# Optimization experiments

Hardware: AMD Instinct MI355X
Metric: run time of the kernel (lower is better)

## Reference

```python
import jax, jax.numpy as jnp
import numpy as np

N = 50000          # nodes
E = 1600000        # edges (avg degree 32)
H, DH = 8, 16      # heads, dim per head (SE3Transformer heads=8, dim_head=16)
D_IN = 8           # pos(3) + node-type embedding(5)
EDGE_DIM = 4       # edge_attr features (num_degrees=4)
HID = H * DH       # 128 = hidden_dim
OUT = 1
TYPES = 100
GRAPHS = 64


def setup_inputs() -> dict:
    key = jax.random.key(0)
    ks = jax.random.split(key, 12)
    pos = jax.random.normal(ks[0], (N, 3), dtype=jnp.float32)
    z = jax.random.randint(ks[1], (N,), 0, TYPES)
    edge_index = jax.random.randint(ks[2], (2, E), 0, N)
    edge_attr = jax.random.normal(ks[3], (E, EDGE_DIM), dtype=jnp.float32)
    batch = jnp.sort(jax.random.randint(ks[4], (N,), 0, GRAPHS))
    s = 0.1
    emb = jax.random.normal(ks[5], (TYPES, D_IN - 3), dtype=jnp.float32) * s
    Wq = jax.random.normal(ks[6], (D_IN, HID), dtype=jnp.float32) * s
    Wk = jax.random.normal(ks[7], (D_IN + EDGE_DIM, HID), dtype=jnp.float32) * s
    Wv = jax.random.normal(ks[8], (D_IN + EDGE_DIM, HID), dtype=jnp.float32) * s
    Wo = jax.random.normal(ks[9], (HID, HID), dtype=jnp.float32) * s
    lin_W = jax.random.normal(ks[10], (HID, OUT), dtype=jnp.float32) * s
    lin_b = jnp.zeros((OUT,), dtype=jnp.float32)
    return {"pos": pos, "z": z, "edge_index": edge_index, "edge_attr": edge_attr,
            "batch": batch, "emb": emb, "Wq": Wq, "Wk": Wk, "Wv": Wv,
            "Wo": Wo, "lin_W": lin_W, "lin_b": lin_b}


def reference(pos, z, edge_index, edge_attr, batch, emb, Wq, Wk, Wv, Wo, lin_W, lin_b):
    # node features: concat(pos, embedding(z))  -> [N, 8]
    x = jnp.concatenate([pos, emb[z]], axis=-1)
    src, dst = edge_index[0], edge_index[1]

    # edge-indexed multi-head graph attention (SE3Transformer core pattern)
    q = (x @ Wq).reshape(N, H, DH)                           # [N, H, DH]
    e_in = jnp.concatenate([x[src], edge_attr], axis=-1)     # [E, 12] gather
    k = (e_in @ Wk).reshape(E, H, DH)
    v = (e_in @ Wv).reshape(E, H, DH)

    scale = 1.0 / jnp.sqrt(jnp.float32(DH))
    scores = jnp.einsum('ehd,ehd->eh', q[dst], k) * scale    # [E, H]

    # segment softmax over incoming edges of each destination node
    m = jax.ops.segment_max(scores, dst, num_segments=N)     # [N, H]
    ex = jnp.exp(scores - m[dst])
    denom = jax.ops.segment_sum(ex, dst, num_segments=N)     # [N, H]
    w = ex / jnp.maximum(denom[dst], 1e-9)                   # [E, H]

    agg = jax.ops.segment_sum(w[:, :, None] * v, dst, num_segments=N)  # [N, H, DH]
    feats = agg.reshape(N, HID) @ Wo                         # [N, 128]

    h = jax.nn.relu(feats)
    y = h @ lin_W + lin_b                                    # [N, OUT]

    # global mean pool per graph
    sums = jax.ops.segment_sum(y, batch, num_segments=GRAPHS)
    cnts = jax.ops.segment_sum(jnp.ones((N, 1), y.dtype), batch, num_segments=GRAPHS)
    return sums / jnp.maximum(cnts, 1.0)                     # [GRAPHS, OUT]
```

## Files before the change

### kernel.cpp

```cpp
#include <hip/hip_runtime.h>

#define N_NODES 50000
#define N_EDGES 1600000
#define NHEAD 8
#define DH 16
#define D_IN 8
#define E_IN_DIM 12
#define HID 128
#define GRAPHS 64
#define N_PAD 50016
#define BINK 98
#define NB 512
#define T_MS 2048
#define MSB ((N_EDGES + T_MS - 1) / T_MS)
#define LCAP 3840

__global__ __launch_bounds__(256) void k_node1(
    const float* __restrict__ pos, const int* __restrict__ z,
    const float* __restrict__ emb,
    const float* __restrict__ Wq, const float* __restrict__ Wk,
    float* __restrict__ x, float* __restrict__ qk)
{
    __shared__ float sWq[D_IN * HID];
    __shared__ float sWk[E_IN_DIM * HID];
    __shared__ float sx[32][D_IN];

    int tid = threadIdx.x;
    for (int i = tid; i < D_IN * HID; i += 256) sWq[i] = Wq[i];
    for (int i = tid; i < E_IN_DIM * HID; i += 256) sWk[i] = Wk[i];

    int nl = tid >> 3;
    int h  = tid & 7;
    int n  = blockIdx.x * 32 + nl;

    if (n < N_NODES) {
        int j = h;
        float v;
        if (j < 3) v = pos[n * 3 + j];
        else       v = emb[z[n] * 5 + (j - 3)];
        sx[nl][j] = v;
        x[n * D_IN + j] = v;
    }
    __syncthreads();
    if (n >= N_NODES) return;

    float q[DH];
    #pragma unroll
    for (int d = 0; d < DH; ++d) {
        float acc = 0.f;
        #pragma unroll
        for (int j = 0; j < D_IN; ++j)
            acc += sx[nl][j] * sWq[j * HID + h * DH + d];
        q[d] = acc;
    }
    const float scale = 0.25f;
    #pragma unroll
    for (int j = 0; j < E_IN_DIM; ++j) {
        float acc = 0.f;
        #pragma unroll
        for (int d = 0; d < DH; ++d)
            acc += q[d] * sWk[j * HID + h * DH + d];
        qk[n * 96 + h * 12 + j] = acc * scale;
    }
}

__global__ __launch_bounds__(256) void k_bhist(
    const int* __restrict__ dst, int* __restrict__ bcount)
{
    __shared__ int lh[NB];
    int tid = threadIdx.x;
    for (int i = tid; i < NB; i += 256) lh[i] = 0;
    __syncthreads();

    int stride = gridDim.x * 256;
    const int NI4 = N_EDGES / 4;
    for (int i = blockIdx.x * 256 + tid; i < NI4; i += stride) {
        int4 d4 = ((const int4*)dst)[i];
        atomicAdd(&lh[d4.x / BINK], 1);
        atomicAdd(&lh[d4.y / BINK], 1);
        atomicAdd(&lh[d4.z / BINK], 1);
        atomicAdd(&lh[d4.w / BINK], 1);
    }
    __syncthreads();
    for (int i = tid; i < NB; i += 256) {
        int v = lh[i];
        if (v > 0) atomicAdd(&bcount[i * 16], v);
    }
}

__global__ __launch_bounds__(512) void k_bscan(
    const int* __restrict__ bcount, int* __restrict__ binoff, int* __restrict__ bincur)
{
    __shared__ int tmp[NB];
    int t = threadIdx.x;
    int v = bcount[t * 16];
    tmp[t] = v;
    __syncthreads();
    #pragma unroll
    for (int off = 1; off < NB; off <<= 1) {
        int u = (t >= off) ? tmp[t - off] : 0;
        __syncthreads();
        if (t >= off) tmp[t] += u;
        __syncthreads();
    }
    int ex = tmp[t] - v;
    binoff[t] = ex;
    bincur[t * 16] = ex;
    if (t == NB - 1) binoff[NB] = tmp[t];
}

__global__ __launch_bounds__(512) void k_msplit(
    const int* __restrict__ edge_index, const float* __restrict__ edge_attr,
    int* __restrict__ bincur,
    int2* __restrict__ sd_g, float4* __restrict__ ea_g)
{
    __shared__ int    hist[NB];
    __shared__ int    hscan[NB];
    __shared__ int    gb[NB];
    __shared__ int2   ssd[T_MS];
    __shared__ float4 sea[T_MS];
    __shared__ int    dest[T_MS];

    int tid = threadIdx.x;
    int base = blockIdx.x * T_MS;
    int nact = min(T_MS, N_EDGES - base);

    hist[tid] = 0;
    __syncthreads();

    int e0 = base + tid * 4;
    bool act = (e0 + 4) <= N_EDGES;
    int srcs[4], dsts[4], myb[4], myr[4];
    float4 eav[4];
    if (act) {
        int4 sa = *(const int4*)(edge_index + e0);
        int4 da = *(const int4*)(edge_index + N_EDGES + e0);
        srcs[0]=sa.x; srcs[1]=sa.y; srcs[2]=sa.z; srcs[3]=sa.w;
        dsts[0]=da.x; dsts[1]=da.y; dsts[2]=da.z; dsts[3]=da.w;
        const float4* ep = (const float4*)edge_attr + e0;
        eav[0] = ep[0]; eav[1] = ep[1]; eav[2] = ep[2]; eav[3] = ep[3];
        #pragma unroll
        for (int k = 0; k < 4; ++k) {
            myb[k] = dsts[k] / BINK;
            myr[k] = atomicAdd(&hist[myb[k]], 1);
        }
    }
    __syncthreads();

    int v = hist[tid];
    hscan[tid] = v;
    __syncthreads();
    #pragma unroll
    for (int off = 1; off < NB; off <<= 1) {
        int u = (tid >= off) ? hscan[tid - off] : 0;
        __syncthreads();
        if (tid >= off) hscan[tid] += u;
        __syncthreads();
    }
    int ex = hscan[tid] - v;
    int g = 0;
    if (v > 0) g = atomicAdd(&bincur[tid * 16], v);
    hscan[tid] = ex;
    gb[tid] = g;
    __syncthreads();

    if (act) {
        #pragma unroll
        for (int k = 0; k < 4; ++k) {
            int li = hscan[myb[k]] + myr[k];
            ssd[li]  = make_int2(srcs[k], dsts[k]);
            sea[li]  = eav[k];
            dest[li] = gb[myb[k]] + myr[k];
        }
    }
    __syncthreads();

    for (int i = tid; i < nact; i += 512) {
        int d = dest[i];
        sd_g[d] = ssd[i];
        ea_g[d] = sea[i];
    }
}

__global__ __launch_bounds__(512) void k_attn_f(
    const int* __restrict__ binoff, const int2* __restrict__ sd_g,
    const float4* __restrict__ ea_g,
    const float* __restrict__ x,
    const float* __restrict__ qk, const float* __restrict__ Wv,
    float* __restrict__ agg)
{
    __shared__ float sWv[E_IN_DIM * HID];
    __shared__ int   soff[129];
    __shared__ int   cnt[BINK];
    __shared__ int   stmp[128];
    __shared__ int2  list[LCAP];

    int tid = threadIdx.x;
    int b = blockIdx.x;
    int nlo = b * BINK;
    int nhi = min(nlo + BINK, N_NODES);
    int nn = nhi - nlo;
    if (nn <= 0) return;

    for (int i = tid; i < E_IN_DIM * HID; i += 512) sWv[i] = Wv[i];
    for (int i = tid; i < nn; i += 512) cnt[i] = 0;
    int gbeg = binoff[b];
    int total = binoff[b + 1] - gbeg;
    __syncthreads();

    for (int i = tid; i < total; i += 512) {
        int2 v = sd_g[gbeg + i];
        atomicAdd(&cnt[v.y - nlo], 1);
    }
    __syncthreads();

    if (tid < 128) stmp[tid] = (tid < nn) ? cnt[tid] : 0;
    __syncthreads();
    #pragma unroll
    for (int off = 1; off < 128; off <<= 1) {
        int u = 0;
        if (tid < 128 && tid >= off) u = stmp[tid - off];
        __syncthreads();
        if (tid < 128 && tid >= off) stmp[tid] += u;
        __syncthreads();
    }
    if (tid < 128) soff[tid + 1] = stmp[tid];
    if (tid == 0) soff[0] = 0;
    for (int i = tid; i < nn; i += 512) cnt[i] = 0;
    __syncthreads();

    for (int i = tid; i < total; i += 512) {
        int2 v = sd_g[gbeg + i];
        int ln = v.y - nlo;
        int r = atomicAdd(&cnt[ln], 1);
        int li = soff[ln] + r;
        if (li < LCAP) list[li] = make_int2(v.x, i);
    }
    __syncthreads();

    int w = tid >> 6, l = tid & 63;
    int es = l >> 3, h = l & 7;
    const float4* easeg = ea_g + gbeg;
    for (int nl = w; nl < nn; nl += 8) {
        int n = nlo + nl;
        const float4* qr = (const float4*)(qk + (size_t)n * 96 + h * 12);
        float4 q0 = qr[0], q1 = qr[1], q2 = qr[2];
        int lbeg = soff[nl];
        int lcnt = soff[nl + 1] - lbeg;

        float sr[12];
        #pragma unroll
        for (int j = 0; j < 12; ++j) sr[j] = 0.f;
        float denom = 0.f;

        int umax = (lcnt + 7) >> 3;
        #pragma unroll 2
        for (int u = 0; u < umax; ++u) {
            int r = u * 8 + es;
            bool a2 = r < lcnt;
            int2 p = list[lbeg + (a2 ? r : 0)];
            const float4* xp = (const float4*)(x + p.x * 8);
            float4 x0 = xp[0], x1 = xp[1];
            float4 ea = easeg[p.y];
            float sc = x0.x*q0.x + x0.y*q0.y + x0.z*q0.z + x0.w*q0.w
                     + x1.x*q1.x + x1.y*q1.y + x1.z*q1.z + x1.w*q1.w
                     + ea.x*q2.x + ea.y*q2.y + ea.z*q2.z + ea.w*q2.w;
            float ex = a2 ? __expf(sc) : 0.f;
            denom += ex;
            sr[0] += ex * x0.x; sr[1]  += ex * x0.y; sr[2]  += ex * x0.z; sr[3]  += ex * x0.w;
            sr[4] += ex * x1.x; sr[5]  += ex * x1.y; sr[6]  += ex * x1.z; sr[7]  += ex * x1.w;
            sr[8] += ex * ea.x; sr[9]  += ex * ea.y; sr[10] += ex * ea.z; sr[11] += ex * ea.w;
        }

        #pragma unroll
        for (int m = 8; m <= 32; m <<= 1) {
            denom += __shfl_xor(denom, m);
            #pragma unroll
            for (int j = 0; j < 12; ++j) sr[j] += __shfl_xor(sr[j], m);
        }

        float inv = 1.0f / fmaxf(denom, 1e-9f);
        int d0 = h * DH + 2 * es;
        float a0 = 0.f, a1 = 0.f;
        #pragma unroll
        for (int j = 0; j < E_IN_DIM; ++j) {
            a0 += sr[j] * sWv[j * HID + d0];
            a1 += sr[j] * sWv[j * HID + d0 + 1];
        }
        *(float2*)(agg + (size_t)n * HID + d0) = make_float2(a0 * inv, a1 * inv);
    }
}

__global__ __launch_bounds__(256) void k_mlp(
    const float* __restrict__ agg, const float* __restrict__ Wo,
    const float* __restrict__ lin_W, const float* __restrict__ lin_b,
    const int* __restrict__ batch,
    float* __restrict__ gsum, float* __restrict__ gcnt)
{
    __shared__ float sWo[64 * HID];
    __shared__ float sAgg[32][HID + 1];
    __shared__ float sRed[8][33];
    __shared__ float bsum[GRAPHS];
    __shared__ int   bcnt[GRAPHS];

    int tid = threadIdx.x;
    int nbase = blockIdx.x * 32;

    if (tid < GRAPHS) { bsum[tid] = 0.f; bcnt[tid] = 0; }

    {
        const float4* ag = (const float4*)(agg + (size_t)nbase * HID);
        #pragma unroll
        for (int k = 0; k < 4; ++k) {
            int i4 = k * 256 + tid;
            float4 v = ag[i4];
            int fi = i4 * 4;
            int r = fi >> 7, c = fi & 127;
            sAgg[r][c] = v.x; sAgg[r][c + 1] = v.y; sAgg[r][c + 2] = v.z; sAgg[r][c + 3] = v.w;
        }
    }

    int h  = tid >> 5;
    int nl = tid & 31;
    int n  = nbase + nl;

    float f[16];
    #pragma unroll
    for (int d = 0; d < 16; ++d) f[d] = 0.f;

    #pragma unroll
    for (int half = 0; half < 2; ++half) {
        __syncthreads();
        const float4* wp = (const float4*)(Wo + half * 64 * HID);
        #pragma unroll
        for (int k = 0; k < 8; ++k) {
            int i4 = k * 256 + tid;
            ((float4*)sWo)[i4] = wp[i4];
        }
        __syncthreads();
        #pragma unroll 4
        for (int i = 0; i < 64; ++i) {
            float av = sAgg[nl][half * 64 + i];
            const float4* wr = (const float4*)(sWo + i * HID + h * 16);
            float4 w0 = wr[0], w1 = wr[1], w2 = wr[2], w3 = wr[3];
            f[0]  += av * w0.x; f[1]  += av * w0.y; f[2]  += av * w0.z; f[3]  += av * w0.w;
            f[4]  += av * w1.x; f[5]  += av * w1.y; f[6]  += av * w1.z; f[7]  += av * w1.w;
            f[8]  += av * w2.x; f[9]  += av * w2.y; f[10] += av * w2.z; f[11] += av * w2.w;
            f[12] += av * w3.x; f[13] += av * w3.y; f[14] += av * w3.z; f[15] += av * w3.w;
        }
    }

    const float4* lwp = (const float4*)(lin_W + h * 16);
    float4 lw0 = lwp[0], lw1 = lwp[1], lw2 = lwp[2], lw3 = lwp[3];
    float ps = fmaxf(f[0],0.f)*lw0.x + fmaxf(f[1],0.f)*lw0.y + fmaxf(f[2],0.f)*lw0.z + fmaxf(f[3],0.f)*lw0.w
             + fmaxf(f[4],0.f)*lw1.x + fmaxf(f[5],0.f)*lw1.y + fmaxf(f[6],0.f)*lw1.z + fmaxf(f[7],0.f)*lw1.w
             + fmaxf(f[8],0.f)*lw2.x + fmaxf(f[9],0.f)*lw2.y + fmaxf(f[10],0.f)*lw2.z + fmaxf(f[11],0.f)*lw2.w
             + fmaxf(f[12],0.f)*lw3.x + fmaxf(f[13],0.f)*lw3.y + fmaxf(f[14],0.f)*lw3.z + fmaxf(f[15],0.f)*lw3.w;

    sRed[h][nl] = ps;
    __syncthreads();
    if (h == 0 && n < N_NODES) {
        float y = lin_b[0];
        #pragma unroll
        for (int k = 0; k < 8; ++k) y += sRed[k][nl];
        int g = batch[n];
        atomicAdd(&bsum[g], y);
        atomicAdd(&bcnt[g], 1);
    }
    __syncthreads();
    if (tid < GRAPHS) {
        int c = bcnt[tid];
        if (c > 0) {
            atomicAdd(&gsum[tid], bsum[tid]);
            atomicAdd(&gcnt[tid], (float)c);
        }
    }
}

__global__ void k_final(const float* __restrict__ gsum, const float* __restrict__ gcnt,
                        float* __restrict__ out)
{
    int g = threadIdx.x;
    if (g < GRAPHS) out[g] = gsum[g] / fmaxf(gcnt[g], 1.0f);
}

extern "C" void kernel_launch(void* const* d_in, const int* in_sizes, int n_in,
                              void* d_out, int out_size, void* d_ws, size_t ws_size,
                              hipStream_t stream)
{
    const float* pos       = (const float*)d_in[0];
    const int*   z         = (const int*)  d_in[1];
    const int*   edge_index= (const int*)  d_in[2];
    const float* edge_attr = (const float*)d_in[3];
    const int*   batch     = (const int*)  d_in[4];
    const float* emb       = (const float*)d_in[5];
    const float* Wq        = (const float*)d_in[6];
    const float* Wk        = (const float*)d_in[7];
    const float* Wv        = (const float*)d_in[8];
    const float* Wo        = (const float*)d_in[9];
    const float* lin_W     = (const float*)d_in[10];
    const float* lin_b     = (const float*)d_in[11];
    float* out = (float*)d_out;

    char* ws = (char*)d_ws;
    float* gsum   = (float*)ws;
    float* gcnt   = gsum + GRAPHS;
    int*   bcount = (int*)(gcnt + GRAPHS);
    int*   binoff = bcount + NB * 16;
    int*   bincur = binoff + 520;
    char*  tail   = (char*)(bincur + NB * 16);

    hipMemsetAsync(gsum, 0, (size_t)(2 * GRAPHS + NB * 16) * sizeof(int), stream);

    int2*   sd_g = (int2*)tail;
    float4* ea_g = (float4*)(sd_g + N_EDGES);
    float*  x    = (float*)(ea_g + N_EDGES);
    float*  qk   = x + (size_t)N_NODES * 8;
    float*  agg  = qk + (size_t)N_NODES * 96;

    k_node1 <<<(N_NODES + 31) / 32, 256, 0, stream>>>(pos, z, emb, Wq, Wk, x, qk);
    k_bhist <<<512, 256, 0, stream>>>(edge_index + N_EDGES, bcount);
    k_bscan <<<1, NB, 0, stream>>>(bcount, binoff, bincur);
    k_msplit<<<MSB, 512, 0, stream>>>(edge_index, edge_attr, bincur, sd_g, ea_g);
    k_attn_f<<<NB, 512, 0, stream>>>(binoff, sd_g, ea_g, x, qk, Wv, agg);
    k_mlp   <<<(N_PAD / 32), 256, 0, stream>>>(agg, Wo, lin_W, lin_b, batch, gsum, gcnt);
    k_final <<<1, 64, 0, stream>>>(gsum, gcnt, out);
}
```

Before: 190.2 us.

## Fuse q·Wk projection into attention kernel and widen blocks to 1024 threads

The per-node q and folded q·Wk vectors are now computed inside the attention kernel, one node per wavefront, instead of a separate node kernel writing a 96-float-per-node qk buffer to global memory. The node kernel shrinks to building x only. The attention kernel grows to 1024 threads with 16 wavefronts, and each thread keeps its edge records in registers between the counting pass and the list-building pass rather than reading them from global memory twice. The trade-off is extra per-node compute and shared-memory/register pressure in the attention kernel. The intra-wave shared-memory exchange relies on wavefront lockstep plus waitcnt rather than a barrier, and the held[4] buffer assumes at most 4096 edges per bin.

```diff
diff --git a/kernel.cpp b/kernel.cpp
--- a/kernel.cpp
+++ b/kernel.cpp
@@ -15,53 +15,18 @@
 #define MSB ((N_EDGES + T_MS - 1) / T_MS)
 #define LCAP 3840
 
-__global__ __launch_bounds__(256) void k_node1(
+__global__ __launch_bounds__(256) void k_nodex(
     const float* __restrict__ pos, const int* __restrict__ z,
-    const float* __restrict__ emb,
-    const float* __restrict__ Wq, const float* __restrict__ Wk,
-    float* __restrict__ x, float* __restrict__ qk)
-{
-    __shared__ float sWq[D_IN * HID];
-    __shared__ float sWk[E_IN_DIM * HID];
-    __shared__ float sx[32][D_IN];
-
-    int tid = threadIdx.x;
-    for (int i = tid; i < D_IN * HID; i += 256) sWq[i] = Wq[i];
-    for (int i = tid; i < E_IN_DIM * HID; i += 256) sWk[i] = Wk[i];
-
-    int nl = tid >> 3;
-    int h  = tid & 7;
-    int n  = blockIdx.x * 32 + nl;
-
-    if (n < N_NODES) {
-        int j = h;
-        float v;
-        if (j < 3) v = pos[n * 3 + j];
-        else       v = emb[z[n] * 5 + (j - 3)];
-        sx[nl][j] = v;
-        x[n * D_IN + j] = v;
-    }
-    __syncthreads();
+    const float* __restrict__ emb, float* __restrict__ x)
+{
+    int n = blockIdx.x * 256 + threadIdx.x;
     if (n >= N_NODES) return;
-
-    float q[DH];
-    #pragma unroll
-    for (int d = 0; d < DH; ++d) {
-        float acc = 0.f;
-        #pragma unroll
-        for (int j = 0; j < D_IN; ++j)
-            acc += sx[nl][j] * sWq[j * HID + h * DH + d];
-        q[d] = acc;
-    }
-    const float scale = 0.25f;
-    #pragma unroll
-    for (int j = 0; j < E_IN_DIM; ++j) {
-        float acc = 0.f;
-        #pragma unroll
-        for (int d = 0; d < DH; ++d)
-            acc += q[d] * sWk[j * HID + h * DH + d];
-        qk[n * 96 + h * 12 + j] = acc * scale;
-    }
+    float p0 = pos[n * 3], p1 = pos[n * 3 + 1], p2 = pos[n * 3 + 2];
+    const float* e = emb + z[n] * 5;
+    float e0 = e[0], e1 = e[1], e2 = e[2], e3 = e[3], e4 = e[4];
+    float4* xp = (float4*)(x + (size_t)n * 8);
+    xp[0] = make_float4(p0, p1, p2, e0);
+    xp[1] = make_float4(e1, e2, e3, e4);
 }
 
 __global__ __launch_bounds__(256) void k_bhist(
@@ -182,18 +147,23 @@
     }
 }
 
-__global__ __launch_bounds__(512) void k_attn_f(
+__global__ __launch_bounds__(1024) void k_attn_f(
     const int* __restrict__ binoff, const int2* __restrict__ sd_g,
     const float4* __restrict__ ea_g,
     const float* __restrict__ x,
-    const float* __restrict__ qk, const float* __restrict__ Wv,
+    const float* __restrict__ Wq, const float* __restrict__ Wk,
+    const float* __restrict__ Wv,
     float* __restrict__ agg)
 {
     __shared__ float sWv[E_IN_DIM * HID];
+    __shared__ float sWq[D_IN * HID];
+    __shared__ float sWk[E_IN_DIM * HID];
     __shared__ int   soff[129];
     __shared__ int   cnt[BINK];
     __shared__ int   stmp[128];
     __shared__ int2  list[LCAP];
+    __shared__ float qsc[16][128];
+    __shared__ float qksc[16][96];
 
     int tid = threadIdx.x;
     int b = blockIdx.x;
@@ -202,15 +172,22 @@
     int nn = nhi - nlo;
     if (nn <= 0) return;
 
-    for (int i = tid; i < E_IN_DIM * HID; i += 512) sWv[i] = Wv[i];
-    for (int i = tid; i < nn; i += 512) cnt[i] = 0;
+    for (int i = tid; i < E_IN_DIM * HID; i += 1024) sWv[i] = Wv[i];
+    for (int i = tid; i < D_IN * HID; i += 1024) sWq[i] = Wq[i];
+    for (int i = tid; i < E_IN_DIM * HID; i += 1024) sWk[i] = Wk[i];
+    for (int i = tid; i < nn; i += 1024) cnt[i] = 0;
     int gbeg = binoff[b];
     int total = binoff[b + 1] - gbeg;
     __syncthreads();
 
-    for (int i = tid; i < total; i += 512) {
-        int2 v = sd_g[gbeg + i];
-        atomicAdd(&cnt[v.y - nlo], 1);
+    int2 held[4];
+    #pragma unroll
+    for (int k = 0; k < 4; ++k) {
+        int i = tid + k * 1024;
+        if (i < total) {
+            held[k] = sd_g[gbeg + i];
+            atomicAdd(&cnt[held[k].y - nlo], 1);
+        }
     }
     __syncthreads();
 
@@ -226,25 +203,61 @@
     }
     if (tid < 128) soff[tid + 1] = stmp[tid];
     if (tid == 0) soff[0] = 0;
-    for (int i = tid; i < nn; i += 512) cnt[i] = 0;
-    __syncthreads();
-
-    for (int i = tid; i < total; i += 512) {
-        int2 v = sd_g[gbeg + i];
-        int ln = v.y - nlo;
-        int r = atomicAdd(&cnt[ln], 1);
-        int li = soff[ln] + r;
-        if (li < LCAP) list[li] = make_int2(v.x, i);
+    for (int i = tid; i < nn; i += 1024) cnt[i] = 0;
+    __syncthreads();
+
+    #pragma unroll
+    for (int k = 0; k < 4; ++k) {
+        int i = tid + k * 1024;
+        if (i < total) {
+            int ln = held[k].y - nlo;
+            int r = atomicAdd(&cnt[ln], 1);
+            int li = soff[ln] + r;
+            if (li < LCAP) list[li] = make_int2(held[k].x, i);
+        }
     }
     __syncthreads();
 
     int w = tid >> 6, l = tid & 63;
     int es = l >> 3, h = l & 7;
     const float4* easeg = ea_g + gbeg;
-    for (int nl = w; nl < nn; nl += 8) {
+    for (int nl = w; nl < nn; nl += 16) {
         int n = nlo + nl;
-        const float4* qr = (const float4*)(qk + (size_t)n * 96 + h * 12);
+
+        {
+            const float4* xp4 = (const float4*)(x + (size_t)n * 8);
+            float4 xa = xp4[0], xb = xp4[1];
+            float xr[8] = {xa.x, xa.y, xa.z, xa.w, xb.x, xb.y, xb.z, xb.w};
+            float qa = 0.f, qb = 0.f;
+            #pragma unroll
+            for (int j = 0; j < 8; ++j) {
+                qa += xr[j] * sWq[j * HID + 2 * l];
+                qb += xr[j] * sWq[j * HID + 2 * l + 1];
+            }
+            qsc[w][2 * l]     = qa;
+            qsc[w][2 * l + 1] = qb;
+            __builtin_amdgcn_s_waitcnt(0);
+            {
+                int e = l, hh = e / 12, jj = e % 12;
+                float acc = 0.f;
+                #pragma unroll
+                for (int d = 0; d < 16; ++d)
+                    acc += qsc[w][hh * 16 + d] * sWk[jj * HID + hh * 16 + d];
+                qksc[w][e] = acc * 0.25f;
+                if (l < 32) {
+                    int e2 = l + 64, h2 = e2 / 12, j2 = e2 % 12;
+                    float acc2 = 0.f;
+                    #pragma unroll
+                    for (int d = 0; d < 16; ++d)
+                        acc2 += qsc[w][h2 * 16 + d] * sWk[j2 * HID + h2 * 16 + d];
+                    qksc[w][e2] = acc2 * 0.25f;
+                }
+            }
+            __builtin_amdgcn_s_waitcnt(0);
+        }
+        const float4* qr = (const float4*)&qksc[w][h * 12];
         float4 q0 = qr[0], q1 = qr[1], q2 = qr[2];
+
         int lbeg = soff[nl];
         int lcnt = soff[nl + 1] - lbeg;
 
@@ -415,14 +428,13 @@
     int2*   sd_g = (int2*)tail;
     float4* ea_g = (float4*)(sd_g + N_EDGES);
     float*  x    = (float*)(ea_g + N_EDGES);
-    float*  qk   = x + (size_t)N_NODES * 8;
-    float*  agg  = qk + (size_t)N_NODES * 96;
-
-    k_node1 <<<(N_NODES + 31) / 32, 256, 0, stream>>>(pos, z, emb, Wq, Wk, x, qk);
+    float*  agg  = x + (size_t)N_NODES * 8;
+
+    k_nodex <<<(N_NODES + 255) / 256, 256, 0, stream>>>(pos, z, emb, x);
     k_bhist <<<512, 256, 0, stream>>>(edge_index + N_EDGES, bcount);
     k_bscan <<<1, NB, 0, stream>>>(bcount, binoff, bincur);
     k_msplit<<<MSB, 512, 0, stream>>>(edge_index, edge_attr, bincur, sd_g, ea_g);
-    k_attn_f<<<NB, 512, 0, stream>>>(binoff, sd_g, ea_g, x, qk, Wv, agg);
+    k_attn_f<<<NB, 1024, 0, stream>>>(binoff, sd_g, ea_g, x, Wq, Wk, Wv, agg);
     k_mlp   <<<(N_PAD / 32), 256, 0, stream>>>(agg, Wo, lin_W, lin_b, batch, gsum, gcnt);
     k_final <<<1, 64, 0, stream>>>(gsum, gcnt, out);
 }
```

Result: no change. 193.0 us (+1.4%).

## Split each attention bin across two blocks and cache edge records in registers

Applied to the files above, without the earlier changes.

The attention kernel now launches two blocks per destination-node bin, each handling half of the bin's nodes (49 nodes) with a smaller shared edge list. Each block scans its parent bin's edges and keeps only the ones landing in its half. Those edge records are held in registers between the counting pass and the list-building pass instead of being read from global memory twice. The aim is more blocks in flight and lower shared memory per block, at the cost of each block reading the whole parent bin. It also assumes no bin holds more than 4096 edges.

```diff
diff --git a/kernel.cpp b/kernel.cpp
--- a/kernel.cpp
+++ b/kernel.cpp
@@ -11,9 +11,11 @@
 #define N_PAD 50016
 #define BINK 98
 #define NB 512
+#define SBK 49
+#define NSUB 1024
 #define T_MS 2048
 #define MSB ((N_EDGES + T_MS - 1) / T_MS)
-#define LCAP 3840
+#define LCAP 2048
 
 __global__ __launch_bounds__(256) void k_node1(
     const float* __restrict__ pos, const int* __restrict__ z,
@@ -190,51 +192,63 @@
     float* __restrict__ agg)
 {
     __shared__ float sWv[E_IN_DIM * HID];
-    __shared__ int   soff[129];
-    __shared__ int   cnt[BINK];
-    __shared__ int   stmp[128];
+    __shared__ int   soff[SBK + 1];
+    __shared__ int   cnt[SBK];
+    __shared__ int   stmp[64];
     __shared__ int2  list[LCAP];
 
     int tid = threadIdx.x;
     int b = blockIdx.x;
-    int nlo = b * BINK;
-    int nhi = min(nlo + BINK, N_NODES);
+    int parent = b >> 1;
+    int nlo = parent * BINK + (b & 1) * SBK;
+    int nhi = min(nlo + SBK, N_NODES);
     int nn = nhi - nlo;
     if (nn <= 0) return;
 
     for (int i = tid; i < E_IN_DIM * HID; i += 512) sWv[i] = Wv[i];
     for (int i = tid; i < nn; i += 512) cnt[i] = 0;
-    int gbeg = binoff[b];
-    int total = binoff[b + 1] - gbeg;
-    __syncthreads();
-
-    for (int i = tid; i < total; i += 512) {
-        int2 v = sd_g[gbeg + i];
-        atomicAdd(&cnt[v.y - nlo], 1);
-    }
-    __syncthreads();
-
-    if (tid < 128) stmp[tid] = (tid < nn) ? cnt[tid] : 0;
-    __syncthreads();
-    #pragma unroll
-    for (int off = 1; off < 128; off <<= 1) {
+    int gbeg = binoff[parent];
+    int total = binoff[parent + 1] - gbeg;
+    __syncthreads();
+
+    int2 held[8];
+    #pragma unroll
+    for (int k = 0; k < 8; ++k) {
+        int i = tid + k * 512;
+        if (i < total) {
+            held[k] = sd_g[gbeg + i];
+            int ln = held[k].y - nlo;
+            if (ln >= 0 && ln < nn) atomicAdd(&cnt[ln], 1);
+        }
+    }
+    __syncthreads();
+
+    if (tid < 64) stmp[tid] = (tid < nn) ? cnt[tid] : 0;
+    __syncthreads();
+    #pragma unroll
+    for (int off = 1; off < 64; off <<= 1) {
         int u = 0;
-        if (tid < 128 && tid >= off) u = stmp[tid - off];
-        __syncthreads();
-        if (tid < 128 && tid >= off) stmp[tid] += u;
-        __syncthreads();
-    }
-    if (tid < 128) soff[tid + 1] = stmp[tid];
+        if (tid < 64 && tid >= off) u = stmp[tid - off];
+        __syncthreads();
+        if (tid < 64 && tid >= off) stmp[tid] += u;
+        __syncthreads();
+    }
+    if (tid < 64) soff[tid + 1] = stmp[tid];
     if (tid == 0) soff[0] = 0;
     for (int i = tid; i < nn; i += 512) cnt[i] = 0;
     __syncthreads();
 
-    for (int i = tid; i < total; i += 512) {
-        int2 v = sd_g[gbeg + i];
-        int ln = v.y - nlo;
-        int r = atomicAdd(&cnt[ln], 1);
-        int li = soff[ln] + r;
-        if (li < LCAP) list[li] = make_int2(v.x, i);
+    #pragma unroll
+    for (int k = 0; k < 8; ++k) {
+        int i = tid + k * 512;
+        if (i < total) {
+            int ln = held[k].y - nlo;
+            if (ln >= 0 && ln < nn) {
+                int r = atomicAdd(&cnt[ln], 1);
+                int li = soff[ln] + r;
+                if (li < LCAP) list[li] = make_int2(held[k].x, i);
+            }
+        }
     }
     __syncthreads();
 
@@ -422,7 +436,7 @@
     k_bhist <<<512, 256, 0, stream>>>(edge_index + N_EDGES, bcount);
     k_bscan <<<1, NB, 0, stream>>>(bcount, binoff, bincur);
     k_msplit<<<MSB, 512, 0, stream>>>(edge_index, edge_attr, bincur, sd_g, ea_g);
-    k_attn_f<<<NB, 512, 0, stream>>>(binoff, sd_g, ea_g, x, qk, Wv, agg);
+    k_attn_f<<<NSUB, 512, 0, stream>>>(binoff, sd_g, ea_g, x, qk, Wv, agg);
     k_mlp   <<<(N_PAD / 32), 256, 0, stream>>>(agg, Wo, lin_W, lin_b, batch, gsum, gcnt);
     k_final <<<1, 64, 0, stream>>>(gsum, gcnt, out);
 }
```

New measurement: 196.3 us. 3.2% more time.

## Enlarge msplit tiles and scatter via LDS permutation instead of staged payload

Applied to the files above, without the earlier changes.

The edge-partition kernel now handles 8192 edges per block with 1024 threads, so each bin's global run per block is longer and fewer atomics hit the global bin cursors. Instead of staging the src/dst and edge_attr payload in LDS, it keeps only dst values plus a 16-bit permutation, then re-reads src and edge_attr from global memory in bin-sorted order when writing. This cuts LDS footprint and should make the global writes more contiguous, at the cost of scattered global re-reads of the payload and fewer, larger blocks.

```diff
diff --git a/kernel.cpp b/kernel.cpp
--- a/kernel.cpp
+++ b/kernel.cpp
@@ -11,7 +11,7 @@
 #define N_PAD 50016
 #define BINK 98
 #define NB 512
-#define T_MS 2048
+#define T_MS 8192
 #define MSB ((N_EDGES + T_MS - 1) / T_MS)
 #define LCAP 3840
 
@@ -109,76 +109,65 @@
     if (t == NB - 1) binoff[NB] = tmp[t];
 }
 
-__global__ __launch_bounds__(512) void k_msplit(
+__global__ __launch_bounds__(1024) void k_msplit(
     const int* __restrict__ edge_index, const float* __restrict__ edge_attr,
     int* __restrict__ bincur,
     int2* __restrict__ sd_g, float4* __restrict__ ea_g)
 {
-    __shared__ int    hist[NB];
-    __shared__ int    hscan[NB];
-    __shared__ int    gb[NB];
-    __shared__ int2   ssd[T_MS];
-    __shared__ float4 sea[T_MS];
-    __shared__ int    dest[T_MS];
+    __shared__ int hist[NB];
+    __shared__ int hscan[NB];
+    __shared__ int cnt[NB];
+    __shared__ int gb[NB];
+    __shared__ int stmp[NB];
+    __shared__ int sdst[T_MS];
+    __shared__ unsigned short perm[T_MS];
 
     int tid = threadIdx.x;
     int base = blockIdx.x * T_MS;
     int nact = min(T_MS, N_EDGES - base);
-
-    hist[tid] = 0;
-    __syncthreads();
-
-    int e0 = base + tid * 4;
-    bool act = (e0 + 4) <= N_EDGES;
-    int srcs[4], dsts[4], myb[4], myr[4];
-    float4 eav[4];
-    if (act) {
-        int4 sa = *(const int4*)(edge_index + e0);
-        int4 da = *(const int4*)(edge_index + N_EDGES + e0);
-        srcs[0]=sa.x; srcs[1]=sa.y; srcs[2]=sa.z; srcs[3]=sa.w;
-        dsts[0]=da.x; dsts[1]=da.y; dsts[2]=da.z; dsts[3]=da.w;
-        const float4* ep = (const float4*)edge_attr + e0;
-        eav[0] = ep[0]; eav[1] = ep[1]; eav[2] = ep[2]; eav[3] = ep[3];
-        #pragma unroll
-        for (int k = 0; k < 4; ++k) {
-            myb[k] = dsts[k] / BINK;
-            myr[k] = atomicAdd(&hist[myb[k]], 1);
-        }
-    }
-    __syncthreads();
-
-    int v = hist[tid];
-    hscan[tid] = v;
-    __syncthreads();
-    #pragma unroll
+    const int* dstp = edge_index + N_EDGES;
+
+    for (int i = tid; i < NB; i += 1024) { hist[i] = 0; cnt[i] = 0; }
+    __syncthreads();
+
+    for (int i = tid; i < nact; i += 1024) {
+        int d = dstp[base + i];
+        sdst[i] = d;
+        atomicAdd(&hist[d / BINK], 1);
+    }
+    __syncthreads();
+
+    if (tid < NB) stmp[tid] = hist[tid];
+    __syncthreads();
     for (int off = 1; off < NB; off <<= 1) {
-        int u = (tid >= off) ? hscan[tid - off] : 0;
-        __syncthreads();
-        if (tid >= off) hscan[tid] += u;
-        __syncthreads();
-    }
-    int ex = hscan[tid] - v;
-    int g = 0;
-    if (v > 0) g = atomicAdd(&bincur[tid * 16], v);
-    hscan[tid] = ex;
-    gb[tid] = g;
-    __syncthreads();
-
-    if (act) {
-        #pragma unroll
-        for (int k = 0; k < 4; ++k) {
-            int li = hscan[myb[k]] + myr[k];
-            ssd[li]  = make_int2(srcs[k], dsts[k]);
-            sea[li]  = eav[k];
-            dest[li] = gb[myb[k]] + myr[k];
-        }
-    }
-    __syncthreads();
-
-    for (int i = tid; i < nact; i += 512) {
-        int d = dest[i];
-        sd_g[d] = ssd[i];
-        ea_g[d] = sea[i];
+        int u = 0;
+        if (tid < NB && tid >= off) u = stmp[tid - off];
+        __syncthreads();
+        if (tid < NB && tid >= off) stmp[tid] += u;
+        __syncthreads();
+    }
+    if (tid < NB) {
+        int v = hist[tid];
+        hscan[tid] = stmp[tid] - v;
+        gb[tid] = (v > 0) ? atomicAdd(&bincur[tid * 16], v) : 0;
+    }
+    __syncthreads();
+
+    for (int i = tid; i < nact; i += 1024) {
+        int b = sdst[i] / BINK;
+        int r = atomicAdd(&cnt[b], 1);
+        perm[hscan[b] + r] = (unsigned short)i;
+    }
+    __syncthreads();
+
+    for (int s = tid; s < nact; s += 1024) {
+        int li = (int)perm[s];
+        int e = base + li;
+        int d = sdst[li];
+        int b = d / BINK;
+        int dest = gb[b] + (s - hscan[b]);
+        sd_g[dest] = make_int2(edge_index[e], d);
+        ea_g[dest] = ((const float4*)edge_attr)[e];
     }
 }
 
@@ -421,7 +410,7 @@
     k_node1 <<<(N_NODES + 31) / 32, 256, 0, stream>>>(pos, z, emb, Wq, Wk, x, qk);
     k_bhist <<<512, 256, 0, stream>>>(edge_index + N_EDGES, bcount);
     k_bscan <<<1, NB, 0, stream>>>(bcount, binoff, bincur);
-    k_msplit<<<MSB, 512, 0, stream>>>(edge_index, edge_attr, bincur, sd_g, ea_g);
+    k_msplit<<<MSB, 1024, 0, stream>>>(edge_index, edge_attr, bincur, sd_g, ea_g);
     k_attn_f<<<NB, 512, 0, stream>>>(binoff, sd_g, ea_g, x, qk, Wv, agg);
     k_mlp   <<<(N_PAD / 32), 256, 0, stream>>>(agg, Wo, lin_W, lin_b, batch, gsum, gcnt);
     k_final <<<1, 64, 0, stream>>>(gsum, gcnt, out);
```

Measured after the change: 182.9 us. 1.04x faster.
